# Kernel optimization log

Measured on AMD Instinct MI355X. Metric: run time of the kernel, lower is better.

## Reference

```python
import jax, jax.numpy as jnp
import numpy as np

SEQ, D_IN, D_H, D_OUT = 8192, 1024, 2048, 1024


def setup_inputs() -> dict:
    key = jax.random.key(0)
    ks = jax.random.split(key, 5)
    # small init scales keep tanh out of full saturation (torch code uses randn,
    # but unit-scale weights would saturate; math is identical regardless of scale)
    return {
        "x_seq": jax.random.normal(ks[0], (SEQ, D_IN), jnp.float32),
        "h0": jnp.zeros((D_H,), jnp.float32),
        "W_ih": jax.random.normal(ks[1], (D_H, D_IN), jnp.float32) / np.sqrt(D_IN),
        "W_hh": jax.random.normal(ks[2], (D_H, D_H), jnp.float32) / np.sqrt(D_H),
        "b_h": jnp.zeros((D_H,), jnp.float32),
        "W_ho_w": jax.random.normal(ks[3], (D_OUT, D_H), jnp.float32) / np.sqrt(D_H),
        "W_ho_b": jnp.zeros((D_OUT,), jnp.float32),
    }


def reference(x_seq, h0, W_ih, W_hh, b_h, W_ho_w, W_ho_b):
    # Precompute the input projection for all steps at once (same math as
    # W_ih @ x_t per step, just batched): (S, H)
    xw = x_seq @ W_ih.T + b_h

    def step(h, xw_t):
        h = jnp.tanh(xw_t + W_hh @ h)  # recurrent matvec + tanh
        return h, h

    h_final, hs = jax.lax.scan(step, h0, xw)  # hs: (S, H)
    outputs = hs @ W_ho_w.T + W_ho_b          # (S, O)
    return outputs, h_final
```

## Files before the change

kernel.cpp:

```cpp
#include <hip/hip_runtime.h>
#include <hip/hip_bf16.h>

#define SEQ   8192
#define DIN   1024
#define DH    2048
#define DOUT  1024

#define SENT 0x7fc0deadu

typedef __attribute__((ext_vector_type(8))) short bf16frag;
typedef __attribute__((ext_vector_type(4))) float f32x4;

__global__ __launch_bounds__(256) void fill_sent_kernel(uint4* __restrict__ p, size_t n4) {
    size_t i = (size_t)blockIdx.x * blockDim.x + threadIdx.x;
    size_t stride = (size_t)gridDim.x * blockDim.x;
    uint4 v = make_uint4(SENT, SENT, SENT, SENT);
    for (; i < n4; i += stride) p[i] = v;
}

static __device__ inline unsigned short f2bf(float f) {
    unsigned u = __float_as_uint(f);
    u += 0x7fffu + ((u >> 16) & 1u);
    return (unsigned short)(u >> 16);
}
__global__ __launch_bounds__(256) void cvt_bf16_kernel(
    const float4* __restrict__ src, ushort4* __restrict__ dst, size_t n4) {
    size_t i = (size_t)blockIdx.x * blockDim.x + threadIdx.x;
    size_t stride = (size_t)gridDim.x * blockDim.x;
    for (; i < n4; i += stride) {
        const float4 v = src[i];
        ushort4 o;
        o.x = f2bf(v.x); o.y = f2bf(v.y); o.z = f2bf(v.z); o.w = f2bf(v.w);
        dst[i] = o;
    }
}

__global__ __launch_bounds__(256) void gemm_nt_bias(
    const float* __restrict__ A, const float* __restrict__ B,
    const float* __restrict__ bias, float* __restrict__ C,
    int M, int N, int K) {
    __shared__ float As[16][132];
    __shared__ float Bs[16][68];
    const int tid = threadIdx.x;
    const int bm = blockIdx.x * 128;
    const int bn = blockIdx.y * 64;
    const int alr = tid >> 1;
    const int alk = (tid & 1) * 8;
    const int blr = tid >> 2;
    const int blk = (tid & 3) * 4;
    const int tm = (tid >> 4) * 8;
    const int tn = (tid & 15) * 4;
    float acc[8][4] = {};

    for (int k0 = 0; k0 < K; k0 += 16) {
        const float4 a0 = *(const float4*)&A[(size_t)(bm + alr) * K + k0 + alk];
        const float4 a1 = *(const float4*)&A[(size_t)(bm + alr) * K + k0 + alk + 4];
        const float4 bv = *(const float4*)&B[(size_t)(bn + blr) * K + k0 + blk];
        As[alk + 0][alr] = a0.x; As[alk + 1][alr] = a0.y;
        As[alk + 2][alr] = a0.z; As[alk + 3][alr] = a0.w;
        As[alk + 4][alr] = a1.x; As[alk + 5][alr] = a1.y;
        As[alk + 6][alr] = a1.z; As[alk + 7][alr] = a1.w;
        Bs[blk + 0][blr] = bv.x; Bs[blk + 1][blr] = bv.y;
        Bs[blk + 2][blr] = bv.z; Bs[blk + 3][blr] = bv.w;
        __syncthreads();
#pragma unroll
        for (int k = 0; k < 16; ++k) {
            const float4 af0 = *(const float4*)&As[k][tm];
            const float4 af1 = *(const float4*)&As[k][tm + 4];
            const float4 bf  = *(const float4*)&Bs[k][tn];
            const float a[8] = {af0.x, af0.y, af0.z, af0.w,
                                af1.x, af1.y, af1.z, af1.w};
            const float b[4] = {bf.x, bf.y, bf.z, bf.w};
#pragma unroll
            for (int i = 0; i < 8; ++i)
#pragma unroll
                for (int j = 0; j < 4; ++j)
                    acc[i][j] = fmaf(a[i], b[j], acc[i][j]);
        }
        __syncthreads();
    }

    const float4 bv = *(const float4*)&bias[bn + tn];
#pragma unroll
    for (int i = 0; i < 8; ++i) {
        float4 o;
        o.x = acc[i][0] + bv.x;
        o.y = acc[i][1] + bv.y;
        o.z = acc[i][2] + bv.z;
        o.w = acc[i][3] + bv.w;
        *(float4*)&C[(size_t)(bm + tm + i) * N + bn + tn] = o;
    }
}

__global__ __launch_bounds__(256) void gemm_bf16_mfma(
    const unsigned short* __restrict__ A, const unsigned short* __restrict__ B,
    const float* __restrict__ bias, float* __restrict__ C,
    int M, int N, int K) {
    const int tid = threadIdx.x;
    const int wave = tid >> 6;
    const int lane = tid & 63;
    const int bm = blockIdx.x * 64 + wave * 16;
    const int bn = blockIdx.y * 64;
    const int r  = lane & 15;
    const int ks = (lane >> 4) * 8;

    f32x4 acc[4] = {};
    const unsigned short* arow = A + (size_t)(bm + r) * K + ks;
    const unsigned short* brow = B + (size_t)(bn + r) * K + ks;

    for (int k0 = 0; k0 < K; k0 += 32) {
        const bf16frag a = *(const bf16frag*)(arow + k0);
#pragma unroll
        for (int ct = 0; ct < 4; ++ct) {
            const bf16frag b = *(const bf16frag*)(brow + (size_t)ct * 16 * K + k0);
            acc[ct] = __builtin_amdgcn_mfma_f32_16x16x32_bf16(a, b, acc[ct], 0, 0, 0);
        }
    }

    const int orow = bm + (lane >> 4) * 4;
#pragma unroll
    for (int ct = 0; ct < 4; ++ct) {
        const int col = bn + ct * 16 + (lane & 15);
        const float bv = bias[col];
#pragma unroll
        for (int i = 0; i < 4; ++i)
            C[(size_t)(orow + i) * N + col] = acc[ct][i] + bv;
    }
}

__global__ __attribute__((amdgpu_flat_work_group_size(512, 512),
                          amdgpu_waves_per_eu(2, 2)))
void rnn_recurrence(
    const float* __restrict__ Whh, const float* __restrict__ xw,
    const float* __restrict__ h0, float* __restrict__ hs) {
    __shared__ float part[2][8][16];
    const int tid = threadIdx.x;
    const int wave = tid >> 6;
    const int lane = tid & 63;
    const int rbase = blockIdx.x * 16;
    const int c0 = 4 * tid;

    float4 w[16];
#pragma unroll
    for (int r = 0; r < 16; ++r) {
        w[r] = *(const float4*)&Whh[(size_t)(rbase + r) * DH + c0];
        asm volatile("" : "+v"(w[r].x), "+v"(w[r].y), "+v"(w[r].z), "+v"(w[r].w));
    }

    for (int t = 0; t < SEQ; ++t) {
        const int par = t & 1;
        float xwv = 0.f;
        if (tid < 16) xwv = xw[(size_t)t * DH + rbase + tid];

        float4 hv;
        if (t == 0) {
            hv = *(const float4*)&h0[c0];
        } else {
            const float* a0 = hs + (size_t)(t - 1) * DH + c0;
            unsigned bad;
            do {
                asm volatile(
                    "global_load_dwordx4 %0, %1, off sc0 sc1\n\t"
                    "s_waitcnt vmcnt(0)"
                    : "=&v"(hv) : "v"(a0) : "memory");
                bad = (__float_as_uint(hv.x) == SENT) | (__float_as_uint(hv.y) == SENT) |
                      (__float_as_uint(hv.z) == SENT) | (__float_as_uint(hv.w) == SENT);
            } while (__builtin_expect(bad != 0, 0));
        }

        float acc[16];
#pragma unroll
        for (int r = 0; r < 16; ++r)
            acc[r] = fmaf(w[r].w, hv.w,
                     fmaf(w[r].z, hv.z,
                     fmaf(w[r].y, hv.y, w[r].x * hv.x)));

        const bool b0 = (lane & 1) != 0, b1 = (lane & 2) != 0,
                   b2 = (lane & 4) != 0, b3 = (lane & 8) != 0;
        float s8[8];
#pragma unroll
        for (int j = 0; j < 8; ++j) {
            const float k = b0 ? acc[2 * j + 1] : acc[2 * j];
            const float g = b0 ? acc[2 * j]     : acc[2 * j + 1];
            s8[j] = k + __shfl_xor(g, 1);
        }
        float s4[4];
#pragma unroll
        for (int j = 0; j < 4; ++j) {
            const float k = b1 ? s8[2 * j + 1] : s8[2 * j];
            const float g = b1 ? s8[2 * j]     : s8[2 * j + 1];
            s4[j] = k + __shfl_xor(g, 2);
        }
        float s2[2];
#pragma unroll
        for (int j = 0; j < 2; ++j) {
            const float k = b2 ? s4[2 * j + 1] : s4[2 * j];
            const float g = b2 ? s4[2 * j]     : s4[2 * j + 1];
            s2[j] = k + __shfl_xor(g, 4);
        }
        float s1;
        {
            const float k = b3 ? s2[1] : s2[0];
            const float g = b3 ? s2[0] : s2[1];
            s1 = k + __shfl_xor(g, 8);
        }
        s1 += __shfl_xor(s1, 16);
        s1 += __shfl_xor(s1, 32);

        if (lane < 16) part[par][wave][lane] = s1;
        __syncthreads();

        if (tid < 16) {
            const float sum =
                part[par][0][tid] + part[par][1][tid] + part[par][2][tid] +
                part[par][3][tid] + part[par][4][tid] + part[par][5][tid] +
                part[par][6][tid] + part[par][7][tid];
            const float hval = tanhf(sum + xwv);
            __hip_atomic_store((unsigned*)(hs + (size_t)t * DH + rbase + tid),
                               __float_as_uint(hval),
                               __ATOMIC_RELAXED, __HIP_MEMORY_SCOPE_AGENT);
        }
    }
}

__global__ __launch_bounds__(256) void copy_hfinal(const float* __restrict__ hs,
                                                   float* __restrict__ out) {
    const int i = blockIdx.x * 256 + threadIdx.x;
    out[i] = hs[(size_t)(SEQ - 1) * DH + i];
}

extern "C" void kernel_launch(void* const* d_in, const int* in_sizes, int n_in,
                              void* d_out, int out_size, void* d_ws, size_t ws_size,
                              hipStream_t stream) {
    (void)in_sizes; (void)n_in; (void)out_size; (void)ws_size;
    const float* x_seq  = (const float*)d_in[0];
    const float* h0     = (const float*)d_in[1];
    const float* W_ih   = (const float*)d_in[2];
    const float* W_hh   = (const float*)d_in[3];
    const float* b_h    = (const float*)d_in[4];
    const float* W_ho_w = (const float*)d_in[5];
    const float* W_ho_b = (const float*)d_in[6];
    float* out = (float*)d_out;

    float* xw = (float*)d_ws;
    float* hs = xw + (size_t)SEQ * DH;
    unsigned short* hsb = (unsigned short*)xw;
    unsigned short* wob = hsb + (size_t)SEQ * DH;

    fill_sent_kernel<<<2048, 256, 0, stream>>>((uint4*)hs, (size_t)SEQ * DH / 4);

    gemm_nt_bias<<<dim3(SEQ / 128, DH / 64), 256, 0, stream>>>(
        x_seq, W_ih, b_h, xw, SEQ, DH, DIN);

    rnn_recurrence<<<DH / 16, 512, 0, stream>>>(W_hh, xw, h0, hs);

    cvt_bf16_kernel<<<2048, 256, 0, stream>>>(
        (const float4*)hs, (ushort4*)hsb, (size_t)SEQ * DH / 4);
    cvt_bf16_kernel<<<1024, 256, 0, stream>>>(
        (const float4*)W_ho_w, (ushort4*)wob, (size_t)DOUT * DH / 4);

    gemm_bf16_mfma<<<dim3(SEQ / 64, DOUT / 64), 256, 0, stream>>>(
        hsb, wob, W_ho_b, out, SEQ, DOUT, DH);

    copy_hfinal<<<DH / 256, 256, 0, stream>>>(hs, out + (size_t)SEQ * DOUT);
}
```

Baseline: 14.38 ms.

## Fuse input-projection GEMM into recurrence kernel with sentinel-polled xw dataflow

Merges the input projection GEMM into the recurrence launch. 128 blocks run the sequential recurrence, and 2048 extra blocks compute xw tiles and publish them with agent-scope atomic stores. The recurrence blocks poll xw for a sentinel value before using it, so the GEMM overlaps the serial recurrence instead of running before it. In exchange, GEMM blocks now use 512-thread blocks with half the threads idle, the sentinel fill covers twice the memory, and correctness depends on the recurrence blocks being resident and on the GEMM finishing tiles in time.

```diff
diff --git a/kernel.cpp b/kernel.cpp
--- a/kernel.cpp
+++ b/kernel.cpp
@@ -32,63 +32,6 @@
         ushort4 o;
         o.x = f2bf(v.x); o.y = f2bf(v.y); o.z = f2bf(v.z); o.w = f2bf(v.w);
         dst[i] = o;
-    }
-}
-
-__global__ __launch_bounds__(256) void gemm_nt_bias(
-    const float* __restrict__ A, const float* __restrict__ B,
-    const float* __restrict__ bias, float* __restrict__ C,
-    int M, int N, int K) {
-    __shared__ float As[16][132];
-    __shared__ float Bs[16][68];
-    const int tid = threadIdx.x;
-    const int bm = blockIdx.x * 128;
-    const int bn = blockIdx.y * 64;
-    const int alr = tid >> 1;
-    const int alk = (tid & 1) * 8;
-    const int blr = tid >> 2;
-    const int blk = (tid & 3) * 4;
-    const int tm = (tid >> 4) * 8;
-    const int tn = (tid & 15) * 4;
-    float acc[8][4] = {};
-
-    for (int k0 = 0; k0 < K; k0 += 16) {
-        const float4 a0 = *(const float4*)&A[(size_t)(bm + alr) * K + k0 + alk];
-        const float4 a1 = *(const float4*)&A[(size_t)(bm + alr) * K + k0 + alk + 4];
-        const float4 bv = *(const float4*)&B[(size_t)(bn + blr) * K + k0 + blk];
-        As[alk + 0][alr] = a0.x; As[alk + 1][alr] = a0.y;
-        As[alk + 2][alr] = a0.z; As[alk + 3][alr] = a0.w;
-        As[alk + 4][alr] = a1.x; As[alk + 5][alr] = a1.y;
-        As[alk + 6][alr] = a1.z; As[alk + 7][alr] = a1.w;
-        Bs[blk + 0][blr] = bv.x; Bs[blk + 1][blr] = bv.y;
-        Bs[blk + 2][blr] = bv.z; Bs[blk + 3][blr] = bv.w;
-        __syncthreads();
-#pragma unroll
-        for (int k = 0; k < 16; ++k) {
-            const float4 af0 = *(const float4*)&As[k][tm];
-            const float4 af1 = *(const float4*)&As[k][tm + 4];
-            const float4 bf  = *(const float4*)&Bs[k][tn];
-            const float a[8] = {af0.x, af0.y, af0.z, af0.w,
-                                af1.x, af1.y, af1.z, af1.w};
-            const float b[4] = {bf.x, bf.y, bf.z, bf.w};
-#pragma unroll
-            for (int i = 0; i < 8; ++i)
-#pragma unroll
-                for (int j = 0; j < 4; ++j)
-                    acc[i][j] = fmaf(a[i], b[j], acc[i][j]);
-        }
-        __syncthreads();
-    }
-
-    const float4 bv = *(const float4*)&bias[bn + tn];
-#pragma unroll
-    for (int i = 0; i < 8; ++i) {
-        float4 o;
-        o.x = acc[i][0] + bv.x;
-        o.y = acc[i][1] + bv.y;
-        o.z = acc[i][2] + bv.z;
-        o.w = acc[i][3] + bv.w;
-        *(float4*)&C[(size_t)(bm + tm + i) * N + bn + tn] = o;
     }
 }
 
@@ -130,11 +73,83 @@
 
 __global__ __attribute__((amdgpu_flat_work_group_size(512, 512),
                           amdgpu_waves_per_eu(2, 2)))
-void rnn_recurrence(
-    const float* __restrict__ Whh, const float* __restrict__ xw,
+void fused_rnn(
+    const float* __restrict__ Whh, float* __restrict__ xw,
+    const float* __restrict__ x_seq, const float* __restrict__ W_ih,
+    const float* __restrict__ b_h,
     const float* __restrict__ h0, float* __restrict__ hs) {
     __shared__ float part[2][8][16];
+    __shared__ float As[16][132];
+    __shared__ float Bs[16][68];
     const int tid = threadIdx.x;
+
+    if (blockIdx.x >= 128) {
+        const int tau = blockIdx.x - 128;
+        const int bm = (tau >> 5) * 128;
+        const int bn = (tau & 31) * 64;
+        const int K = DIN, N = DH;
+        const int alr = tid >> 1;
+        const int alk = (tid & 1) * 8;
+        const int blr = tid >> 2;
+        const int blk = (tid & 3) * 4;
+        const int tm = (tid >> 4) * 8;
+        const int tn = (tid & 15) * 4;
+        float acc[8][4] = {};
+
+        for (int k0 = 0; k0 < K; k0 += 16) {
+            if (tid < 256) {
+                const float4 a0 = *(const float4*)&x_seq[(size_t)(bm + alr) * K + k0 + alk];
+                const float4 a1 = *(const float4*)&x_seq[(size_t)(bm + alr) * K + k0 + alk + 4];
+                const float4 bv = *(const float4*)&W_ih[(size_t)(bn + blr) * K + k0 + blk];
+                As[alk + 0][alr] = a0.x; As[alk + 1][alr] = a0.y;
+                As[alk + 2][alr] = a0.z; As[alk + 3][alr] = a0.w;
+                As[alk + 4][alr] = a1.x; As[alk + 5][alr] = a1.y;
+                As[alk + 6][alr] = a1.z; As[alk + 7][alr] = a1.w;
+                Bs[blk + 0][blr] = bv.x; Bs[blk + 1][blr] = bv.y;
+                Bs[blk + 2][blr] = bv.z; Bs[blk + 3][blr] = bv.w;
+            }
+            __syncthreads();
+            if (tid < 256) {
+#pragma unroll
+                for (int k = 0; k < 16; ++k) {
+                    const float4 af0 = *(const float4*)&As[k][tm];
+                    const float4 af1 = *(const float4*)&As[k][tm + 4];
+                    const float4 bf  = *(const float4*)&Bs[k][tn];
+                    const float a[8] = {af0.x, af0.y, af0.z, af0.w,
+                                        af1.x, af1.y, af1.z, af1.w};
+                    const float b[4] = {bf.x, bf.y, bf.z, bf.w};
+#pragma unroll
+                    for (int i = 0; i < 8; ++i)
+#pragma unroll
+                        for (int j = 0; j < 4; ++j)
+                            acc[i][j] = fmaf(a[i], b[j], acc[i][j]);
+                }
+            }
+            __syncthreads();
+        }
+
+        if (tid < 256) {
+            const float4 bv = *(const float4*)&b_h[bn + tn];
+#pragma unroll
+            for (int i = 0; i < 8; ++i) {
+                const float o0 = acc[i][0] + bv.x;
+                const float o1 = acc[i][1] + bv.y;
+                const float o2 = acc[i][2] + bv.z;
+                const float o3 = acc[i][3] + bv.w;
+                unsigned* dst = (unsigned*)&xw[(size_t)(bm + tm + i) * N + bn + tn];
+                __hip_atomic_store(dst + 0, __float_as_uint(o0),
+                                   __ATOMIC_RELAXED, __HIP_MEMORY_SCOPE_AGENT);
+                __hip_atomic_store(dst + 1, __float_as_uint(o1),
+                                   __ATOMIC_RELAXED, __HIP_MEMORY_SCOPE_AGENT);
+                __hip_atomic_store(dst + 2, __float_as_uint(o2),
+                                   __ATOMIC_RELAXED, __HIP_MEMORY_SCOPE_AGENT);
+                __hip_atomic_store(dst + 3, __float_as_uint(o3),
+                                   __ATOMIC_RELAXED, __HIP_MEMORY_SCOPE_AGENT);
+            }
+        }
+        return;
+    }
+
     const int wave = tid >> 6;
     const int lane = tid & 63;
     const int rbase = blockIdx.x * 16;
@@ -149,8 +164,12 @@
 
     for (int t = 0; t < SEQ; ++t) {
         const int par = t & 1;
+
         float xwv = 0.f;
-        if (tid < 16) xwv = xw[(size_t)t * DH + rbase + tid];
+        const float* xaddr = xw + (size_t)t * DH + rbase + tid;
+        if (tid < 16)
+            asm volatile("global_load_dword %0, %1, off sc0 sc1"
+                         : "=&v"(xwv) : "v"(xaddr) : "memory");
 
         float4 hv;
         if (t == 0) {
@@ -211,6 +230,14 @@
         __syncthreads();
 
         if (tid < 16) {
+            asm volatile("s_waitcnt vmcnt(0)" ::: "memory");
+            __builtin_amdgcn_sched_barrier(0);
+            while (__builtin_expect(__float_as_uint(xwv) == SENT, 0)) {
+                asm volatile(
+                    "global_load_dword %0, %1, off sc0 sc1\n\t"
+                    "s_waitcnt vmcnt(0)"
+                    : "=&v"(xwv) : "v"(xaddr) : "memory");
+            }
             const float sum =
                 part[par][0][tid] + part[par][1][tid] + part[par][2][tid] +
                 part[par][3][tid] + part[par][4][tid] + part[par][5][tid] +
@@ -247,12 +274,11 @@
     unsigned short* hsb = (unsigned short*)xw;
     unsigned short* wob = hsb + (size_t)SEQ * DH;
 
-    fill_sent_kernel<<<2048, 256, 0, stream>>>((uint4*)hs, (size_t)SEQ * DH / 4);
-
-    gemm_nt_bias<<<dim3(SEQ / 128, DH / 64), 256, 0, stream>>>(
-        x_seq, W_ih, b_h, xw, SEQ, DH, DIN);
-
-    rnn_recurrence<<<DH / 16, 512, 0, stream>>>(W_hh, xw, h0, hs);
+    fill_sent_kernel<<<4096, 256, 0, stream>>>((uint4*)xw,
+                                               (size_t)2 * SEQ * DH / 4);
+
+    fused_rnn<<<128 + 2048, 512, 0, stream>>>(W_hh, xw, x_seq, W_ih, b_h,
+                                              h0, hs);
 
     cvt_bf16_kernel<<<2048, 256, 0, stream>>>(
         (const float4*)hs, (ushort4*)hsb, (size_t)SEQ * DH / 4);
```

New measurement: 14.35 ms. Within noise of the previous version (-0.2%).
